# Kernel tuning notes

Hardware: AMD Instinct MI355X
Metric: run time of the kernel (lower is better)

Reference implementation:

```python
import jax, jax.numpy as jnp
import numpy as np

T_STEP = 0.01
N_STEPS = 1000
H_S = 64
N_TARGETS = 2048
INPUT_S = 2
H_NN = 256
ACTION_S = 2


def setup_inputs() -> dict:
    key = jax.random.key(0)
    ks = jax.random.split(key, 9)
    target = jax.random.normal(ks[0], (N_TARGETS, INPUT_S), dtype=jnp.float32)
    D = jax.random.normal(ks[1], (H_S,), dtype=jnp.float32) * 0.1
    P = jax.random.normal(ks[2], (H_S, H_S), dtype=jnp.float32)
    l1_w = jax.random.normal(ks[3], (H_NN, INPUT_S), dtype=jnp.float32) * 0.05
    l1_b = jax.random.normal(ks[4], (H_NN,), dtype=jnp.float32) * 0.05
    l2_w = jax.random.normal(ks[5], (H_S, H_NN), dtype=jnp.float32) * 0.05
    l2_b = jax.random.normal(ks[6], (H_S,), dtype=jnp.float32) * 0.05
    lm_w = jax.random.normal(ks[7], (ACTION_S, H_S), dtype=jnp.float32) * 0.05
    lm_b = jax.random.normal(ks[8], (ACTION_S,), dtype=jnp.float32) * 0.05
    return {"target": target, "D": D, "P": P,
            "l1_w": l1_w, "l1_b": l1_b, "l2_w": l2_w, "l2_b": l2_b,
            "lm_w": lm_w, "lm_b": lm_b}


def reference(target, D, P, l1_w, l1_b, l2_w, l2_b, lm_w, lm_b):
    # initial condition MLP: relu(l1) -> l2, then transpose to (h_s, n_targets)
    h = jax.nn.relu(target @ l1_w.T + l1_b)           # (n_targets, h_nn)
    x0 = (h @ l2_w.T + l2_b).T                        # (h_s, n_targets)
    # A = P diag(exp(D)) P^-1 ; step map x <- (I - dt*A) x
    A = (P * jnp.exp(D)[None, :]) @ jnp.linalg.inv(P)  # (h_s, h_s)
    M = jnp.eye(H_S, dtype=A.dtype) - T_STEP * A

    def step(x, _):
        act = jnp.tanh(x.T @ lm_w.T + lm_b)            # (n_targets, action_s)
        return M @ x, (x, act)

    _, (hidden_states, acts) = jax.lax.scan(step, x0, None, length=N_STEPS)
    # hidden_states: (n_steps, h_s, n_targets); acts: (n_steps, n_targets, action_s)
    actions = jnp.transpose(acts, (1, 2, 0))           # (n_targets, action_s, n_steps)
    return actions, hidden_states
```

## Files before the change

kernel.cpp:

```cpp
#include <hip/hip_runtime.h>
#include <math.h>

#define NT 2048
#define HS 64
#define HNN 256
#define NSTEPS 1000
#define TSTEP 0.01f

typedef unsigned short u16;
typedef __attribute__((ext_vector_type(8))) short bf16x8;
typedef __attribute__((ext_vector_type(4))) float f32x4;

#define OFF_HT   148736

#define S_H 1028

__device__ inline void bsplit(float x, u16& hi, u16& lo) {
    unsigned u = __float_as_uint(x);
    unsigned r = (u + 0x7FFFu + ((u >> 16) & 1u)) >> 16;
    hi = (u16)r;
    float xh = __uint_as_float(r << 16);
    float d = x - xh;
    unsigned v = __float_as_uint(d);
    unsigned s = (v + 0x7FFFu + ((v >> 16) & 1u)) >> 16;
    lo = (u16)s;
}

__device__ inline void bar_lds() {
    asm volatile("s_waitcnt lgkmcnt(0)" ::: "memory");
    __builtin_amdgcn_s_barrier();
    asm volatile("" ::: "memory");
}

__device__ inline float tanh_fast(float x) {
    float xc = fminf(fmaxf(x, -15.f), 15.f);
    float a = __builtin_amdgcn_exp2f(xc * 2.885390082f);
    return (a - 1.f) * __builtin_amdgcn_rcpf(a + 1.f);
}

struct FrontSh {
    union {
        float Aug[64 * 130];
        struct {
            union { float shT[256 * 17]; float rs[64 * 17]; float us[16 * 128]; } a;
            float x0s[64 * 17];
            float y0s[64 * 17];
        } p2;
    } u;
    float Rs[64 * 65];
    float fvec[2][64];
    float tgt[16][2];
    float lam_s[64], l2l_s[64];
    float Q_s[128];
};

__global__ __launch_bounds__(512) void k_front(const float* __restrict__ target,
                                               const float* __restrict__ l1_w,
                                               const float* __restrict__ l1_b,
                                               const float* __restrict__ l2_w,
                                               const float* __restrict__ l2_b,
                                               const float* __restrict__ lm_w,
                                               const float* __restrict__ lm_b,
                                               const float* __restrict__ D,
                                               const float* __restrict__ P,
                                               float* __restrict__ ws,
                                               float* __restrict__ actions) {
    __shared__ FrontSh sh;
    int ct = blockIdx.x;
    int cbase = ct * 16;
    int tid = threadIdx.x;
    float* Aug = sh.u.Aug;

    for (int idx = tid; idx < 64 * 128; idx += 512) {
        int r = idx >> 7, c = idx & 127;
        Aug[r * 130 + c] = (c < 64) ? P[r * 64 + c] : ((c - 64) == r ? 1.f : 0.f);
    }
    __syncthreads();

    if (tid < 64) {
        float nv = Aug[tid * 130];
        float pv = __shfl(nv, 0);
        sh.fvec[0][tid] = (tid == 0) ? 0.f : nv * __builtin_amdgcn_rcpf(pv);
    } else if (tid < 128) {
        int i = tid - 64;
        float l = 1.0f - TSTEP * expf(D[i]);
        sh.lam_s[i] = l;
        sh.l2l_s[i] = log2f(l);
    } else if (tid < 256) {
        int t = tid - 128;
        int a = t >> 6, i = t & 63;
        float s = 0.f;
        for (int r = 0; r < 64; ++r) s = fmaf(lm_w[a * 64 + r], P[r * 64 + i], s);
        sh.Q_s[t] = s;
    } else if (tid < 272) {
        int c = tid - 256;
        float2 tv = ((const float2*)target)[cbase + c];
        sh.tgt[c][0] = tv.x; sh.tgt[c][1] = tv.y;
    }
    __syncthreads();

    for (int t = 0; t < 64; ++t) {
        int par = t & 1;
        if (tid < 64) {
            int col0 = (t < 63) ? (t + 1) : 64;
            float f = sh.fvec[par][tid];
            float src = Aug[t * 130 + col0];
            float nv = Aug[tid * 130 + col0] - f * src;
            Aug[tid * 130 + col0] = nv;
            if (t < 63) {
                float pv = __shfl(nv, t + 1);
                sh.fvec[par ^ 1][tid] = (tid == (t + 1)) ? 0.f
                                        : nv * __builtin_amdgcn_rcpf(pv);
            }
        } else {
            int w = (tid >> 6) - 1;
            int lane = tid & 63;
            float f = sh.fvec[par][lane];
            const float* rowp = Aug + t * 130;
            float* rowr = Aug + lane * 130;
            int pcnt = 63 - t;
            for (int s = 1 + w; s < 64; s += 7) {
                int col = (s < pcnt) ? (t + 1 + s) : (64 + (s - pcnt));
                rowr[col] -= f * rowp[col];
            }
        }
        __syncthreads();
    }

    for (int idx = tid; idx < 4096; idx += 512) {
        int j = idx >> 6, m = idx & 63;
        sh.Rs[j * 65 + m] = Aug[j * 130 + 64 + m]
                            * __builtin_amdgcn_rcpf(Aug[j * 130 + j]);
    }
    __syncthreads();

    if (tid < 256) {
        float w0 = l1_w[2 * tid], w1 = l1_w[2 * tid + 1], bb = l1_b[tid];
        #pragma unroll
        for (int cc = 0; cc < 16; ++cc)
            sh.u.p2.a.shT[tid * 17 + cc] =
                fmaxf(fmaf(w0, sh.tgt[cc][0], fmaf(w1, sh.tgt[cc][1], bb)), 0.f);
    }
    __syncthreads();

    int i = tid >> 3, cs = (tid & 7) * 2;
    {
        const float* l2wi = l2_w + i * 256;
        float bb = l2_b[i];
        float a0 = bb, a1 = bb;
        #pragma unroll 4
        for (int j = 0; j < 256; ++j) {
            float w = l2wi[j];
            a0 = fmaf(w, sh.u.p2.a.shT[j * 17 + cs], a0);
            a1 = fmaf(w, sh.u.p2.a.shT[j * 17 + cs + 1], a1);
        }
        sh.u.p2.x0s[i * 17 + cs] = a0; sh.u.p2.x0s[i * 17 + cs + 1] = a1;
    }
    __syncthreads();

    const float* Ri = sh.Rs + i * 65;
    {
        float b0 = 0, b1 = 0;
        #pragma unroll 4
        for (int m = 0; m < 64; ++m) {
            float rv = Ri[m];
            b0 = fmaf(rv, sh.u.p2.x0s[m * 17 + cs], b0);
            b1 = fmaf(rv, sh.u.p2.x0s[m * 17 + cs + 1], b1);
        }
        sh.u.p2.y0s[i * 17 + cs] = b0; sh.u.p2.y0s[i * 17 + cs + 1] = b1;
    }
    __syncthreads();

    const float* Pi = P + i * 64;
    #pragma unroll 1
    for (int it = 0; it < 2; ++it) {
        float r0 = sh.u.p2.x0s[i * 17 + cs], r1 = sh.u.p2.x0s[i * 17 + cs + 1];
        #pragma unroll 4
        for (int m = 0; m < 64; ++m) {
            float pv = Pi[m];
            r0 = fmaf(-pv, sh.u.p2.y0s[m * 17 + cs], r0);
            r1 = fmaf(-pv, sh.u.p2.y0s[m * 17 + cs + 1], r1);
        }
        __syncthreads();
        sh.u.p2.a.rs[i * 17 + cs] = r0; sh.u.p2.a.rs[i * 17 + cs + 1] = r1;
        __syncthreads();
        float d0 = 0, d1 = 0;
        #pragma unroll 4
        for (int m = 0; m < 64; ++m) {
            float rv = Ri[m];
            d0 = fmaf(rv, sh.u.p2.a.rs[m * 17 + cs], d0);
            d1 = fmaf(rv, sh.u.p2.a.rs[m * 17 + cs + 1], d1);
        }
        sh.u.p2.y0s[i * 17 + cs] += d0; sh.u.p2.y0s[i * 17 + cs + 1] += d1;
        __syncthreads();
    }

    for (int idx = tid; idx < 2048; idx += 512) {
        int cgi = idx >> 7, t = idx & 127;
        sh.u.p2.a.us[cgi * 128 + t] = sh.Q_s[t] * sh.u.p2.y0s[(t & 63) * 17 + cgi];
    }
    if (tid < 128) {
        int kt = tid >> 6, lane = tid & 63;
        int c_l = lane & 15;
        int i0 = kt * 32 + (lane >> 4) * 8;
        u16* YH = (u16*)(ws + OFF_HT);
        u16* YL = YH + 131072;
        bf16x8 vh, vl;
        #pragma unroll
        for (int j = 0; j < 8; ++j) {
            u16 h, lo;
            bsplit(sh.u.p2.y0s[(i0 + j) * 17 + c_l], h, lo);
            vh[j] = (short)h; vl[j] = (short)lo;
        }
        int off = ((ct * 2 + kt) * 64 + lane);
        *(bf16x8*)(YH + off * 8) = vh;
        *(bf16x8*)(YL + off * 8) = vl;
    }
    __syncthreads();

    if (tid < 500) {
        int k0 = tid * 2;
        float b0 = lm_b[0], b1 = lm_b[1];
        float fk0 = (float)k0;
        #pragma unroll 1
        for (int ch = 0; ch < 4; ++ch) {
            int cg0 = ch * 4;
            float2 s[4][2];
            #pragma unroll
            for (int j = 0; j < 4; ++j) {
                s[j][0] = make_float2(b0, b0);
                s[j][1] = make_float2(b1, b1);
            }
            #pragma unroll 4
            for (int ii = 0; ii < 64; ++ii) {
                float p0 = __builtin_amdgcn_exp2f(fk0 * sh.l2l_s[ii]);
                float p1 = p0 * sh.lam_s[ii];
                #pragma unroll
                for (int j = 0; j < 4; ++j) {
                    float u0 = sh.u.p2.a.us[(cg0 + j) * 128 + ii];
                    float u1 = sh.u.p2.a.us[(cg0 + j) * 128 + 64 + ii];
                    s[j][0].x = fmaf(u0, p0, s[j][0].x);
                    s[j][0].y = fmaf(u0, p1, s[j][0].y);
                    s[j][1].x = fmaf(u1, p0, s[j][1].x);
                    s[j][1].y = fmaf(u1, p1, s[j][1].y);
                }
            }
            #pragma unroll
            for (int j = 0; j < 4; ++j)
                #pragma unroll
                for (int a = 0; a < 2; ++a) {
                    float2 r;
                    r.x = tanh_fast(s[j][a].x);
                    r.y = tanh_fast(s[j][a].y);
                    *(float2*)(actions + (size_t)(cbase + cg0 + j) * 2000 + a * 1000 + k0) = r;
                }
        }
    }
}

__global__ __launch_bounds__(512, 2) void k_hidden(const float* __restrict__ P,
                                                   const float* __restrict__ D,
                                                   const float* __restrict__ ws,
                                                   float* __restrict__ hidden) {
    int k = blockIdx.x;
    int tid = threadIdx.x;
    int wid = tid >> 6, lane = tid & 63;
    int l15 = lane & 15, lg = lane >> 4;

    extern __shared__ float stage[];
    __shared__ float lp_s[64];

    const u16* YH = (const u16*)(ws + OFF_HT);
    const u16* YL = YH + 131072;

    if (tid < 64) {
        float l = 1.0f - TSTEP * expf(D[tid]);
        lp_s[tid] = exp2f((float)k * log2f(l));
    }
    __syncthreads();

    bf16x8 ah[4][2], al[4][2];
    #pragma unroll
    for (int rt = 0; rt < 4; ++rt) {
        int r = rt * 16 + l15;
        #pragma unroll
        for (int kt = 0; kt < 2; ++kt) {
            int i0 = kt * 32 + lg * 8;
            #pragma unroll
            for (int j = 0; j < 8; ++j) {
                float v = P[r * 64 + i0 + j] * lp_s[i0 + j];
                u16 h, lo;
                bsplit(v, h, lo);
                ah[rt][kt][j] = (short)h;
                al[rt][kt][j] = (short)lo;
            }
        }
    }

    float* outk = hidden + (size_t)k * 64 * NT;

    #pragma unroll 1
    for (int half = 0; half < 2; ++half) {
        bf16x8 bh[8][2], bl[8][2];
        #pragma unroll
        for (int q = 0; q < 8; ++q)
            #pragma unroll
            for (int kt = 0; kt < 2; ++kt) {
                int ct_g = half * 64 + wid * 8 + q;
                int off = ((ct_g * 2 + kt) * 64 + lane) * 8;
                bh[q][kt] = *(const bf16x8*)(YH + off);
                bl[q][kt] = *(const bf16x8*)(YL + off);
            }
        #pragma unroll
        for (int rt = 0; rt < 4; ++rt) {
            #pragma unroll
            for (int q = 0; q < 8; ++q) {
                f32x4 acc = {0.f, 0.f, 0.f, 0.f};
                #pragma unroll
                for (int kt = 0; kt < 2; ++kt) {
                    acc = __builtin_amdgcn_mfma_f32_16x16x32_bf16(ah[rt][kt], bh[q][kt], acc, 0, 0, 0);
                    acc = __builtin_amdgcn_mfma_f32_16x16x32_bf16(al[rt][kt], bh[q][kt], acc, 0, 0, 0);
                    acc = __builtin_amdgcn_mfma_f32_16x16x32_bf16(ah[rt][kt], bl[q][kt], acc, 0, 0, 0);
                }
                int col = wid * 128 + q * 16 + l15;
                #pragma unroll
                for (int reg = 0; reg < 4; ++reg)
                    stage[(lg * 4 + reg) * S_H + col] = acc[reg];
            }
            bar_lds();
            #pragma unroll
            for (int it = 0; it < 8; ++it) {
                int f = it * 512 + tid;
                int r = f >> 8, c4 = f & 255;
                float4 v = *(const float4*)&stage[r * S_H + (c4 << 2)];
                *(float4*)(outk + (size_t)(rt * 16 + r) * NT + half * 1024 + (c4 << 2)) = v;
            }
            bar_lds();
        }
    }
}

extern "C" void kernel_launch(void* const* d_in, const int* in_sizes, int n_in,
                              void* d_out, int out_size, void* d_ws, size_t ws_size,
                              hipStream_t stream) {
    const float* target = (const float*)d_in[0];
    const float* D      = (const float*)d_in[1];
    const float* P      = (const float*)d_in[2];
    const float* l1_w   = (const float*)d_in[3];
    const float* l1_b   = (const float*)d_in[4];
    const float* l2_w   = (const float*)d_in[5];
    const float* l2_b   = (const float*)d_in[6];
    const float* lm_w   = (const float*)d_in[7];
    const float* lm_b   = (const float*)d_in[8];
    float* ws = (float*)d_ws;
    float* actions = (float*)d_out;
    float* hidden  = (float*)d_out + 4096000;

    hipFuncSetAttribute((const void*)k_hidden,
                        hipFuncAttributeMaxDynamicSharedMemorySize, 16 * S_H * 4);

    hipLaunchKernelGGL(k_front,  dim3(128),  dim3(512), 0, stream,
                       target, l1_w, l1_b, l2_w, l2_b, lm_w, lm_b, D, P, ws, actions);
    hipLaunchKernelGGL(k_hidden, dim3(1000), dim3(512), 16 * S_H * 4, stream, P, D, ws, hidden);
}
```

Baseline: 203.0 us.

## Halve targets per front block to launch 256 blocks and split accumulators

The front kernel now handles 8 targets per block instead of 16 and launches 256 blocks, so more CUs work on the actions computation. Each thread now owns one target column and uses several independent partial accumulators in the small matvecs to shorten dependency chains. The costs are that the 64x64 Gauss-Jordan inverse is recomputed by twice as many blocks, and the bf16 split-store is partitioned by block parity so two blocks each fill half of a 16-column tile.

```diff
diff --git a/kernel.cpp b/kernel.cpp
--- a/kernel.cpp
+++ b/kernel.cpp
@@ -42,14 +42,14 @@
     union {
         float Aug[64 * 130];
         struct {
-            union { float shT[256 * 17]; float rs[64 * 17]; float us[16 * 128]; } a;
+            union { float shT[256 * 17]; float rs[64 * 17]; float us[8 * 128]; } a;
             float x0s[64 * 17];
             float y0s[64 * 17];
         } p2;
     } u;
     float Rs[64 * 65];
     float fvec[2][64];
-    float tgt[16][2];
+    float tgt[8][2];
     float lam_s[64], l2l_s[64];
     float Q_s[128];
 };
@@ -67,7 +67,7 @@
                                                float* __restrict__ actions) {
     __shared__ FrontSh sh;
     int ct = blockIdx.x;
-    int cbase = ct * 16;
+    int cbase = ct * 8;
     int tid = threadIdx.x;
     float* Aug = sh.u.Aug;
 
@@ -92,7 +92,7 @@
         float s = 0.f;
         for (int r = 0; r < 64; ++r) s = fmaf(lm_w[a * 64 + r], P[r * 64 + i], s);
         sh.Q_s[t] = s;
-    } else if (tid < 272) {
+    } else if (tid < 264) {
         int c = tid - 256;
         float2 tv = ((const float2*)target)[cbase + c];
         sh.tgt[c][0] = tv.x; sh.tgt[c][1] = tv.y;
@@ -137,24 +137,24 @@
     if (tid < 256) {
         float w0 = l1_w[2 * tid], w1 = l1_w[2 * tid + 1], bb = l1_b[tid];
         #pragma unroll
-        for (int cc = 0; cc < 16; ++cc)
+        for (int cc = 0; cc < 8; ++cc)
             sh.u.p2.a.shT[tid * 17 + cc] =
                 fmaxf(fmaf(w0, sh.tgt[cc][0], fmaf(w1, sh.tgt[cc][1], bb)), 0.f);
     }
     __syncthreads();
 
-    int i = tid >> 3, cs = (tid & 7) * 2;
+    int i = tid >> 3, c = tid & 7;
     {
         const float* l2wi = l2_w + i * 256;
-        float bb = l2_b[i];
-        float a0 = bb, a1 = bb;
+        float a0 = l2_b[i], a1 = 0, a2 = 0, a3 = 0;
         #pragma unroll 4
-        for (int j = 0; j < 256; ++j) {
-            float w = l2wi[j];
-            a0 = fmaf(w, sh.u.p2.a.shT[j * 17 + cs], a0);
-            a1 = fmaf(w, sh.u.p2.a.shT[j * 17 + cs + 1], a1);
-        }
-        sh.u.p2.x0s[i * 17 + cs] = a0; sh.u.p2.x0s[i * 17 + cs + 1] = a1;
+        for (int j = 0; j < 256; j += 4) {
+            a0 = fmaf(l2wi[j],     sh.u.p2.a.shT[j * 17 + c],       a0);
+            a1 = fmaf(l2wi[j + 1], sh.u.p2.a.shT[(j + 1) * 17 + c], a1);
+            a2 = fmaf(l2wi[j + 2], sh.u.p2.a.shT[(j + 2) * 17 + c], a2);
+            a3 = fmaf(l2wi[j + 3], sh.u.p2.a.shT[(j + 3) * 17 + c], a3);
+        }
+        sh.u.p2.x0s[i * 17 + c] = (a0 + a1) + (a2 + a3);
     }
     __syncthreads();
 
@@ -162,59 +162,59 @@
     {
         float b0 = 0, b1 = 0;
         #pragma unroll 4
-        for (int m = 0; m < 64; ++m) {
-            float rv = Ri[m];
-            b0 = fmaf(rv, sh.u.p2.x0s[m * 17 + cs], b0);
-            b1 = fmaf(rv, sh.u.p2.x0s[m * 17 + cs + 1], b1);
-        }
-        sh.u.p2.y0s[i * 17 + cs] = b0; sh.u.p2.y0s[i * 17 + cs + 1] = b1;
+        for (int m = 0; m < 64; m += 2) {
+            b0 = fmaf(Ri[m],     sh.u.p2.x0s[m * 17 + c],       b0);
+            b1 = fmaf(Ri[m + 1], sh.u.p2.x0s[(m + 1) * 17 + c], b1);
+        }
+        sh.u.p2.y0s[i * 17 + c] = b0 + b1;
     }
     __syncthreads();
 
     const float* Pi = P + i * 64;
     #pragma unroll 1
     for (int it = 0; it < 2; ++it) {
-        float r0 = sh.u.p2.x0s[i * 17 + cs], r1 = sh.u.p2.x0s[i * 17 + cs + 1];
+        float r0 = sh.u.p2.x0s[i * 17 + c], r1 = 0;
         #pragma unroll 4
-        for (int m = 0; m < 64; ++m) {
-            float pv = Pi[m];
-            r0 = fmaf(-pv, sh.u.p2.y0s[m * 17 + cs], r0);
-            r1 = fmaf(-pv, sh.u.p2.y0s[m * 17 + cs + 1], r1);
+        for (int m = 0; m < 64; m += 2) {
+            r0 = fmaf(-Pi[m],     sh.u.p2.y0s[m * 17 + c],       r0);
+            r1 = fmaf(-Pi[m + 1], sh.u.p2.y0s[(m + 1) * 17 + c], r1);
         }
         __syncthreads();
-        sh.u.p2.a.rs[i * 17 + cs] = r0; sh.u.p2.a.rs[i * 17 + cs + 1] = r1;
+        sh.u.p2.a.rs[i * 17 + c] = r0 + r1;
         __syncthreads();
         float d0 = 0, d1 = 0;
         #pragma unroll 4
-        for (int m = 0; m < 64; ++m) {
-            float rv = Ri[m];
-            d0 = fmaf(rv, sh.u.p2.a.rs[m * 17 + cs], d0);
-            d1 = fmaf(rv, sh.u.p2.a.rs[m * 17 + cs + 1], d1);
-        }
-        sh.u.p2.y0s[i * 17 + cs] += d0; sh.u.p2.y0s[i * 17 + cs + 1] += d1;
+        for (int m = 0; m < 64; m += 2) {
+            d0 = fmaf(Ri[m],     sh.u.p2.a.rs[m * 17 + c],       d0);
+            d1 = fmaf(Ri[m + 1], sh.u.p2.a.rs[(m + 1) * 17 + c], d1);
+        }
+        sh.u.p2.y0s[i * 17 + c] += d0 + d1;
         __syncthreads();
     }
 
-    for (int idx = tid; idx < 2048; idx += 512) {
+    for (int idx = tid; idx < 1024; idx += 512) {
         int cgi = idx >> 7, t = idx & 127;
         sh.u.p2.a.us[cgi * 128 + t] = sh.Q_s[t] * sh.u.p2.y0s[(t & 63) * 17 + cgi];
     }
     if (tid < 128) {
         int kt = tid >> 6, lane = tid & 63;
-        int c_l = lane & 15;
-        int i0 = kt * 32 + (lane >> 4) * 8;
-        u16* YH = (u16*)(ws + OFF_HT);
-        u16* YL = YH + 131072;
-        bf16x8 vh, vl;
-        #pragma unroll
-        for (int j = 0; j < 8; ++j) {
-            u16 h, lo;
-            bsplit(sh.u.p2.y0s[(i0 + j) * 17 + c_l], h, lo);
-            vh[j] = (short)h; vl[j] = (short)lo;
-        }
-        int off = ((ct * 2 + kt) * 64 + lane);
-        *(bf16x8*)(YH + off * 8) = vh;
-        *(bf16x8*)(YL + off * 8) = vl;
+        int c15 = lane & 15;
+        if ((c15 >> 3) == (ct & 1)) {
+            int cl = c15 & 7;
+            int i0 = kt * 32 + (lane >> 4) * 8;
+            u16* YH = (u16*)(ws + OFF_HT);
+            u16* YL = YH + 131072;
+            bf16x8 vh, vl;
+            #pragma unroll
+            for (int j = 0; j < 8; ++j) {
+                u16 h, lo;
+                bsplit(sh.u.p2.y0s[(i0 + j) * 17 + cl], h, lo);
+                vh[j] = (short)h; vl[j] = (short)lo;
+            }
+            int off = (((ct >> 1) * 2 + kt) * 64 + lane);
+            *(bf16x8*)(YH + off * 8) = vh;
+            *(bf16x8*)(YL + off * 8) = vl;
+        }
     }
     __syncthreads();
 
@@ -222,39 +222,35 @@
         int k0 = tid * 2;
         float b0 = lm_b[0], b1 = lm_b[1];
         float fk0 = (float)k0;
-        #pragma unroll 1
-        for (int ch = 0; ch < 4; ++ch) {
-            int cg0 = ch * 4;
-            float2 s[4][2];
-            #pragma unroll
-            for (int j = 0; j < 4; ++j) {
-                s[j][0] = make_float2(b0, b0);
-                s[j][1] = make_float2(b1, b1);
-            }
-            #pragma unroll 4
-            for (int ii = 0; ii < 64; ++ii) {
-                float p0 = __builtin_amdgcn_exp2f(fk0 * sh.l2l_s[ii]);
-                float p1 = p0 * sh.lam_s[ii];
-                #pragma unroll
-                for (int j = 0; j < 4; ++j) {
-                    float u0 = sh.u.p2.a.us[(cg0 + j) * 128 + ii];
-                    float u1 = sh.u.p2.a.us[(cg0 + j) * 128 + 64 + ii];
-                    s[j][0].x = fmaf(u0, p0, s[j][0].x);
-                    s[j][0].y = fmaf(u0, p1, s[j][0].y);
-                    s[j][1].x = fmaf(u1, p0, s[j][1].x);
-                    s[j][1].y = fmaf(u1, p1, s[j][1].y);
-                }
-            }
-            #pragma unroll
-            for (int j = 0; j < 4; ++j)
-                #pragma unroll
-                for (int a = 0; a < 2; ++a) {
-                    float2 r;
-                    r.x = tanh_fast(s[j][a].x);
-                    r.y = tanh_fast(s[j][a].y);
-                    *(float2*)(actions + (size_t)(cbase + cg0 + j) * 2000 + a * 1000 + k0) = r;
-                }
-        }
+        float2 s[8][2];
+        #pragma unroll
+        for (int j = 0; j < 8; ++j) {
+            s[j][0] = make_float2(b0, b0);
+            s[j][1] = make_float2(b1, b1);
+        }
+        #pragma unroll 2
+        for (int ii = 0; ii < 64; ++ii) {
+            float p0 = __builtin_amdgcn_exp2f(fk0 * sh.l2l_s[ii]);
+            float p1 = p0 * sh.lam_s[ii];
+            #pragma unroll
+            for (int j = 0; j < 8; ++j) {
+                float u0 = sh.u.p2.a.us[j * 128 + ii];
+                float u1 = sh.u.p2.a.us[j * 128 + 64 + ii];
+                s[j][0].x = fmaf(u0, p0, s[j][0].x);
+                s[j][0].y = fmaf(u0, p1, s[j][0].y);
+                s[j][1].x = fmaf(u1, p0, s[j][1].x);
+                s[j][1].y = fmaf(u1, p1, s[j][1].y);
+            }
+        }
+        #pragma unroll
+        for (int j = 0; j < 8; ++j)
+            #pragma unroll
+            for (int a = 0; a < 2; ++a) {
+                float2 r;
+                r.x = tanh_fast(s[j][a].x);
+                r.y = tanh_fast(s[j][a].y);
+                *(float2*)(actions + (size_t)(cbase + j) * 2000 + a * 1000 + k0) = r;
+            }
     }
 }
 
@@ -359,7 +355,7 @@
     hipFuncSetAttribute((const void*)k_hidden,
                         hipFuncAttributeMaxDynamicSharedMemorySize, 16 * S_H * 4);
 
-    hipLaunchKernelGGL(k_front,  dim3(128),  dim3(512), 0, stream,
+    hipLaunchKernelGGL(k_front,  dim3(256),  dim3(512), 0, stream,
                        target, l1_w, l1_b, l2_w, l2_b, lm_w, lm_b, D, P, ws, actions);
     hipLaunchKernelGGL(k_hidden, dim3(1000), dim3(512), 16 * S_H * 4, stream, P, D, ws, hidden);
 }
```

After: 185.2 us. 1.1x faster.
